# Performance work log

Measured on AMD Instinct MI355X. Metric: run time of the kernel, lower is better.

## Reference

```python
import jax, jax.numpy as jnp
import numpy as np

# ---- module hyperparameters (from init_kwargs) ----
KL_TEMP = 4.0
NUM_CLASSES = 100
POLICY_NUMS = 7          # linear out dim = POLICY_NUMS + 2 (identity, classes, policies)
FEATURE_NUMS = 128       # linear in dim = concat of two 64-d policy features
POS_W = (1.0, 0.5, 0.001)
NEG_W = (1.0, 0.5, 0.001)
KD_CE_W = (1.0, 1.0)
LOSS_W = (1.0, 1.0, 1.0)
BATCH = 2048


def setup_inputs() -> dict:
    key = jax.random.key(0)
    ks = jax.random.split(key, 9)
    O = POLICY_NUMS + 2
    return {
        "student_logits": jax.random.normal(ks[0], (BATCH, NUM_CLASSES), jnp.float32),
        "teacher_logits": jax.random.normal(ks[1], (BATCH, NUM_CLASSES), jnp.float32),
        "student_policy": jax.random.normal(ks[2], (BATCH, FEATURE_NUMS // 2), jnp.float32),
        "teacher_policy": jax.random.normal(ks[3], (BATCH, FEATURE_NUMS // 2), jnp.float32),
        "W1": jax.random.normal(ks[4], (O, FEATURE_NUMS), jnp.float32) * 0.08,  # frozen teacher linear
        "bias1": jax.random.normal(ks[5], (O,), jnp.float32) * 0.01,
        "W2": jax.random.normal(ks[6], (O, FEATURE_NUMS), jnp.float32) * 0.08,  # trainable student linear
        "bias2": jax.random.normal(ks[7], (O,), jnp.float32) * 0.01,
        "targets": jax.random.randint(ks[8], (BATCH, 1, POLICY_NUMS + 1), 0, 10, dtype=jnp.int32),
    }


def _kldiv_mean(inp, tgt):
    # torch KLDivLoss(reduction='mean'): mean over all elems of target*(log(target)-input), zero where target<=0
    safe = jnp.where(tgt > 0, tgt, 1.0)
    return jnp.where(tgt > 0, tgt * (jnp.log(safe) - inp), 0.0).mean()


def _wmean(loss, tgt, pw, nw):
    return jnp.where(tgt == 1.0, loss * pw, loss * nw).mean()


def _pair_linear(feat, W, bias):
    # L[i, j] = W @ concat(f_even[j], f_odd[i]) + bias, computed without materializing [b1,b1,2f]
    f = feat.shape[-1]
    f1, f2 = feat[0::2], feat[1::2]                       # [b1, f] each
    A = f1 @ W[:, :f].T                                   # [b1, O]  (j part)
    B = f2 @ W[:, f:].T                                   # [b1, O]  (i part)
    return B[:, None, :] + A[None, :, :] + bias           # [b1, b1, O]


def _policy_loss(teacher_policy, student_policy, targets, W1, bias1, W2, bias2):
    B = student_policy.shape[0]
    b1 = B // 2
    dt = student_policy.dtype

    Ls = _pair_linear(student_policy, W2, bias2)          # [b1,b1,O]
    Lt = jax.lax.stop_gradient(_pair_linear(teacher_policy, W1, bias1))

    sI, sC = Ls[..., 0], Ls[..., 1]
    sP = Ls[..., 2:].reshape(b1 * b1, POLICY_NUMS)
    tI, tC = Lt[..., 0], Lt[..., 1]
    tP = Lt[..., 2:].reshape(b1 * b1, POLICY_NUMS)

    eye = jnp.eye(b1, dtype=dt)
    # off-diagonal identity entries are detached for the student (teacher already no-grad)
    sI = eye * sI + (1.0 - eye) * jax.lax.stop_gradient(sI)

    t = targets.reshape(B, POLICY_NUMS + 1)
    t1, t2 = t[0::2], t[1::2]
    Teq = (t1[None, :, :] == t2[:, None, :]).astype(dt)   # [b1,b1,P+1]

    classes_value = 1.0 / (NUM_CLASSES - 1) + 1.0
    identity_value = 1.0 / (b1 - 1) + 1.0
    gC = Teq[..., 0] * classes_value - 1.0 / (NUM_CLASSES - 1)
    gP = Teq[..., 1:].reshape(b1 * b1, POLICY_NUMS) * 2.0 - 1.0
    gI = eye * identity_value - 1.0 / (b1 - 1)

    kl_loss = (_wmean((sI - tI) ** 2, gI, POS_W[0], NEG_W[0])
               + _wmean((sC - tC) ** 2, gC, POS_W[1], NEG_W[1])
               + _wmean((sP - tP) ** 2, gP, POS_W[2], NEG_W[2]))

    # KLDivLoss(reduction='mean') returns a scalar; torch.where broadcasts it, so .mean() of weights scales it
    ce_loss = (_kldiv_mean(sI, gI) * jnp.where(gI == 1.0, POS_W[0], NEG_W[0]).mean()
               + _kldiv_mean(sC, gC) * jnp.where(gC == 1.0, POS_W[1], NEG_W[1]).mean()
               + _wmean((sP - gP) ** 2, gP, POS_W[2], NEG_W[2]))

    return KD_CE_W[0] * kl_loss + KD_CE_W[1] * ce_loss


def reference(student_logits, teacher_logits, student_policy, teacher_policy, W1, bias1, W2, bias2, targets):
    B = student_logits.shape[0]
    # ---- CE loss (targets last dim <= 15 -> integer class label at column 0) ----
    labels = targets.reshape(B, -1)[:, 0]
    logp = jax.nn.log_softmax(student_logits, axis=1)
    ce_loss = -jnp.take_along_axis(logp, labels[:, None], axis=1).mean()

    # ---- KD KL loss (KLDivLoss reduction='mean' over all elements) ----
    t_prob = jax.nn.softmax(teacher_logits / KL_TEMP, axis=1)
    s_logp = jax.nn.log_softmax(student_logits / KL_TEMP, axis=1)
    kl_loss = _kldiv_mean(s_logp, t_prob) * (KL_TEMP ** 2)

    # ---- pairwise policy loss (the fusion-heavy path) ----
    policy_loss = _policy_loss(teacher_policy, student_policy, targets, W1, bias1, W2, bias2)

    return LOSS_W[0] * ce_loss + LOSS_W[1] * kl_loss + LOSS_W[2] * policy_loss
```

## Files before the change

### kernel.cpp

```cpp
#include <hip/hip_runtime.h>
#include <math.h>

#define NCLS   100
#define BATCH_ 2048
#define OK     9
#define FHALF  64

#define NLOGB  128
#define NPOLB  16
#define NBLK   (NLOGB + NPOLB)

#define LP_OFF 0
#define PS_OFF (LP_OFF + NLOGB * 2)
#define PB_OFF (PS_OFF + NPOLB * 72)

__device__ __forceinline__ float waveSum(float v) {
#pragma unroll
    for (int off = 32; off; off >>= 1) v += __shfl_xor(v, off, 64);
    return v;
}
__device__ __forceinline__ float waveMax(float v) {
#pragma unroll
    for (int off = 32; off; off >>= 1) v = fmaxf(v, __shfl_xor(v, off, 64));
    return v;
}

__global__ __launch_bounds__(1024) void stats_kernel(
        const float* __restrict__ slog, const float* __restrict__ tlog,
        const float* __restrict__ spol, const float* __restrict__ tpol,
        const float* __restrict__ W1,   const float* __restrict__ W2,
        const int*   __restrict__ tgt,  float* __restrict__ ws)
{
    __shared__ float w1s[OK * 128];
    __shared__ float w2s[OK * 128];
    __shared__ float bkt[320];
    __shared__ float redL[32];

    const int tid  = threadIdx.x;
    const int wave = tid >> 6;
    const int lane = tid & 63;

    if (blockIdx.x < NLOGB) {
        const int r = blockIdx.x * 16 + wave;
        const float* x = slog + r * NCLS;
        const float* y = tlog + r * NCLS;
        const int label = tgt[r * 8];
        const bool has2 = lane < (NCLS - 64);
        float x1 = x[lane];
        float y1 = y[lane];
        float x2 = has2 ? x[lane + 64] : -3.0e38f;
        float y2 = has2 ? y[lane + 64] : -3.0e38f;
        float xl = x[label];
        float mx = waveMax(fmaxf(x1, x2));
        float my = waveMax(fmaxf(y1, y2));
        float se1  = waveSum(expf(x1 - mx) + (has2 ? expf(x2 - mx) : 0.f));
        float se4s = waveSum(expf((x1 - mx) * 0.25f) + (has2 ? expf((x2 - mx) * 0.25f) : 0.f));
        float e1 = expf((y1 - my) * 0.25f);
        float e2 = has2 ? expf((y2 - my) * 0.25f) : 0.f;
        float se4t = waveSum(e1 + e2);
        float tnum = waveSum(e1 * (y1 - x1) * 0.25f + (has2 ? e2 * (y2 - x2) * 0.25f : 0.f));
        if (lane == 0) {
            float logZ1  = mx + logf(se1);
            float logZ4s = mx * 0.25f + logf(se4s);
            float logZ4t = my * 0.25f + logf(se4t);
            redL[wave * 2]     = logZ1 - xl;
            redL[wave * 2 + 1] = tnum / se4t + logZ4s - logZ4t;
        }
        __syncthreads();
        if (tid < 2) {
            float s = 0.f;
#pragma unroll
            for (int w = 0; w < 16; ++w) s += redL[w * 2 + tid];
            ws[LP_OFF + blockIdx.x * 2 + tid] = s;
        }
    } else {
        const int pb = blockIdx.x - NLOGB;
        for (int idx = tid; idx < OK * 128; idx += 1024) { w1s[idx] = W1[idx]; w2s[idx] = W2[idx]; }
        if (tid < 320) bkt[tid] = 0.f;
        __syncthreads();

        float As[OK], Bs[OK];
        if (tid < 64) {
            const int i = pb * 64 + tid;
            const float4* f1s = (const float4*)(spol + (2 * i) * FHALF);
            const float4* f2s = (const float4*)(spol + (2 * i + 1) * FHALF);
            const float4* f1t = (const float4*)(tpol + (2 * i) * FHALF);
            const float4* f2t = (const float4*)(tpol + (2 * i + 1) * FHALF);

            float At[OK], Bt[OK];
#pragma unroll
            for (int k = 0; k < OK; ++k) { As[k] = 0.f; Bs[k] = 0.f; At[k] = 0.f; Bt[k] = 0.f; }
            for (int f4 = 0; f4 < FHALF / 4; ++f4) {
                float4 a4 = f1s[f4], b4 = f2s[f4], c4 = f1t[f4], d4 = f2t[f4];
                const float* ap = (const float*)&a4;
                const float* bp = (const float*)&b4;
                const float* cp = (const float*)&c4;
                const float* dp = (const float*)&d4;
#pragma unroll
                for (int j = 0; j < 4; ++j) {
                    const int f = f4 * 4 + j;
                    const float av = ap[j], bv = bp[j], cv = cp[j], dv = dp[j];
#pragma unroll
                    for (int k = 0; k < OK; ++k) {
                        As[k] = fmaf(av, w2s[k * 128 + f],      As[k]);
                        Bs[k] = fmaf(bv, w2s[k * 128 + 64 + f], Bs[k]);
                        At[k] = fmaf(cv, w1s[k * 128 + f],      At[k]);
                        Bt[k] = fmaf(dv, w1s[k * 128 + 64 + f], Bt[k]);
                    }
                }
            }

#pragma unroll
            for (int k = 0; k < OK; ++k) {
                float du = Bs[k] - Bt[k], dw = As[k] - At[k];
                float v0 = waveSum(du),     v1 = waveSum(du * du);
                float v2 = waveSum(dw),     v3 = waveSum(dw * dw);
                float v4 = waveSum(Bs[k]),  v5 = waveSum(Bs[k] * Bs[k]);
                float v6 = waveSum(As[k]),  v7 = waveSum(As[k] * As[k]);
                if (lane == 0) {
                    float* p = ws + PS_OFF + pb * 72 + k * 8;
                    p[0] = v0; p[1] = v1; p[2] = v2; p[3] = v3;
                    p[4] = v4; p[5] = v5; p[6] = v6; p[7] = v7;
                }
            }

            const int* t1r = tgt + (2 * i) * 8;
            const int* t2r = tgt + (2 * i + 1) * 8;
#pragma unroll
            for (int c0 = 0; c0 < 8; ++c0) {
                int v1i = t1r[c0], v2i = t2r[c0];
                atomicAdd(&bkt[0 * 80 + c0 * 10 + v1i], 1.0f);
                atomicAdd(&bkt[1 * 80 + c0 * 10 + v2i], 1.0f);
                atomicAdd(&bkt[2 * 80 + c0 * 10 + v1i], As[c0 + 1]);
                atomicAdd(&bkt[3 * 80 + c0 * 10 + v2i], Bs[c0 + 1]);
            }
        }
        __syncthreads();
        if (tid < 320) ws[PB_OFF + pb * 320 + tid] = bkt[tid];
    }
}

__global__ __launch_bounds__(256) void combine_kernel(
        const float* __restrict__ ws,
        const float* __restrict__ bias1, const float* __restrict__ bias2,
        float* __restrict__ out)
{
    __shared__ float statsC[72];
    __shared__ float bktC[320];
    __shared__ float cekl[8];

    const int tid  = threadIdx.x;
    const int wave = tid >> 6;
    const int lane = tid & 63;

    float ce = 0.f, kl = 0.f;
    if (tid < NLOGB) {
        ce = ws[LP_OFF + tid * 2];
        kl = ws[LP_OFF + tid * 2 + 1];
    }
    ce = waveSum(ce); kl = waveSum(kl);
    if (lane == 0) { cekl[wave * 2] = ce; cekl[wave * 2 + 1] = kl; }

    if (tid < 72) {
        float s = 0.f;
#pragma unroll
        for (int b = 0; b < NPOLB; ++b) s += ws[PS_OFF + b * 72 + tid];
        statsC[tid] = s;
    }
    for (int idx = tid; idx < 320; idx += 256) {
        float s = 0.f;
#pragma unroll
        for (int b = 0; b < NPOLB; ++b) s += ws[PB_OFF + b * 320 + idx];
        bktC[idx] = s;
    }
    __syncthreads();

    if (tid == 0) {
        const double N = 1024.0, M = 1048576.0;
        double ce_main = (double)(cekl[0] + cekl[2] + cekl[4] + cekl[6]) / (double)BATCH_;
        double kl_main = (double)(cekl[1] + cekl[3] + cekl[5] + cekl[7]) * 16.0
                       / (double)(BATCH_ * NCLS);

        double kl_pol = 0.0, Sp_acc = 0.0;
        double SumL[OK], SumL2[OK];
        for (int k = 0; k < OK; ++k) {
            const float* p = &statsC[k * 8];
            double D1u = p[0], D2u = p[1], D1w = p[2], D2w = p[3];
            double U1 = p[4], U2 = p[5], Wa1 = p[6], Wa2 = p[7];
            double cd = (double)bias2[k] - (double)bias1[k];
            double b  = (double)bias2[k];
            double S = N * D2u + N * (D2w + 2.0 * cd * D1w + N * cd * cd)
                     + 2.0 * D1u * (D1w + N * cd);
            if (k == 0)      kl_pol += S / M;
            else if (k == 1) kl_pol += 0.5 * S / M;
            else             Sp_acc += S;
            SumL[k]  = N * U1 + N * Wa1 + M * b;
            SumL2[k] = N * U2 + N * (Wa2 + 2.0 * b * Wa1 + N * b * b)
                     + 2.0 * U1 * (Wa1 + N * b);
        }
        kl_pol += 0.001 * Sp_acc / (7.0 * M);

        double ce_I = -((double)statsC[4] + (double)statsC[6] + N * (double)bias2[0]) / M;

        const float* cnt1 = &bktC[0];
        const float* cnt2 = &bktC[80];
        const float* sA   = &bktC[160];
        const float* sB   = &bktC[240];
        double ce_C = 0.0, ceP = 0.0;
        for (int c0 = 0; c0 < 8; ++c0) {
            double ms = 0.0, pc = 0.0;
            for (int v = 0; v < 10; ++v) {
                double c1 = (double)cnt1[c0 * 10 + v], c2 = (double)cnt2[c0 * 10 + v];
                ms += c1 * (double)sB[c0 * 10 + v] + c2 * (double)sA[c0 * 10 + v];
                pc += c1 * c2;
            }
            ms += (double)bias2[c0 + 1] * pc;
            if (c0 == 0) {
                ce_C = -0.5 * ms / M;
            } else {
                int k = c0 + 1;
                double sg = 2.0 * ms - SumL[k];
                ceP += SumL2[k] - 2.0 * sg + M;
            }
        }
        ceP *= 0.001 / (7.0 * M);

        out[0] = (float)(ce_main + kl_main + kl_pol + ce_I + ce_C + ceP);
    }
}

extern "C" void kernel_launch(void* const* d_in, const int* in_sizes, int n_in,
                              void* d_out, int out_size, void* d_ws, size_t ws_size,
                              hipStream_t stream) {
    const float* slog = (const float*)d_in[0];
    const float* tlog = (const float*)d_in[1];
    const float* spol = (const float*)d_in[2];
    const float* tpol = (const float*)d_in[3];
    const float* W1   = (const float*)d_in[4];
    const float* b1   = (const float*)d_in[5];
    const float* W2   = (const float*)d_in[6];
    const float* b2   = (const float*)d_in[7];
    const int*   tgt  = (const int*)d_in[8];
    float* ws = (float*)d_ws;

    stats_kernel<<<NBLK, 1024, 0, stream>>>(slog, tlog, spol, tpol, W1, W2, tgt, ws);
    combine_kernel<<<1, 256, 0, stream>>>(ws, b1, b2, (float*)d_out);
}
```

Baseline: 98.07 us.

## Shrink stats blocks to 256 threads and use all threads in policy blocks

Changes the stats kernel from 1024-thread to 256-thread blocks. Logit blocks go from 128 to 512 with four rows each, and policy blocks go from 16 to 4 with every thread computing a pair projection instead of only the first wave. Per-wave projection statistics are reduced in shared memory before the global write, and the combine kernel is adjusted for the larger number of logit partials. This removes the idle 960 threads per policy block and spreads the logit work over more CUs, at the cost of heavier shared-memory atomic contention per policy block.

```diff
diff --git a/kernel.cpp b/kernel.cpp
--- a/kernel.cpp
+++ b/kernel.cpp
@@ -6,8 +6,8 @@
 #define OK     9
 #define FHALF  64
 
-#define NLOGB  128
-#define NPOLB  16
+#define NLOGB  512
+#define NPOLB  4
 #define NBLK   (NLOGB + NPOLB)
 
 #define LP_OFF 0
@@ -25,7 +25,7 @@
     return v;
 }
 
-__global__ __launch_bounds__(1024) void stats_kernel(
+__global__ __launch_bounds__(256) void stats_kernel(
         const float* __restrict__ slog, const float* __restrict__ tlog,
         const float* __restrict__ spol, const float* __restrict__ tpol,
         const float* __restrict__ W1,   const float* __restrict__ W2,
@@ -34,14 +34,15 @@
     __shared__ float w1s[OK * 128];
     __shared__ float w2s[OK * 128];
     __shared__ float bkt[320];
-    __shared__ float redL[32];
+    __shared__ float statsW[4][72];
+    __shared__ float redL[8];
 
     const int tid  = threadIdx.x;
     const int wave = tid >> 6;
     const int lane = tid & 63;
 
     if (blockIdx.x < NLOGB) {
-        const int r = blockIdx.x * 16 + wave;
+        const int r = blockIdx.x * 4 + wave;
         const float* x = slog + r * NCLS;
         const float* y = tlog + r * NCLS;
         const int label = tgt[r * 8];
@@ -67,76 +68,74 @@
             redL[wave * 2 + 1] = tnum / se4t + logZ4s - logZ4t;
         }
         __syncthreads();
-        if (tid < 2) {
-            float s = 0.f;
-#pragma unroll
-            for (int w = 0; w < 16; ++w) s += redL[w * 2 + tid];
-            ws[LP_OFF + blockIdx.x * 2 + tid] = s;
-        }
+        if (tid < 2)
+            ws[LP_OFF + blockIdx.x * 2 + tid] =
+                redL[tid] + redL[2 + tid] + redL[4 + tid] + redL[6 + tid];
     } else {
         const int pb = blockIdx.x - NLOGB;
-        for (int idx = tid; idx < OK * 128; idx += 1024) { w1s[idx] = W1[idx]; w2s[idx] = W2[idx]; }
-        if (tid < 320) bkt[tid] = 0.f;
+        for (int idx = tid; idx < OK * 128; idx += 256) { w1s[idx] = W1[idx]; w2s[idx] = W2[idx]; }
+        for (int idx = tid; idx < 320; idx += 256) bkt[idx] = 0.f;
         __syncthreads();
 
-        float As[OK], Bs[OK];
-        if (tid < 64) {
-            const int i = pb * 64 + tid;
-            const float4* f1s = (const float4*)(spol + (2 * i) * FHALF);
-            const float4* f2s = (const float4*)(spol + (2 * i + 1) * FHALF);
-            const float4* f1t = (const float4*)(tpol + (2 * i) * FHALF);
-            const float4* f2t = (const float4*)(tpol + (2 * i + 1) * FHALF);
-
-            float At[OK], Bt[OK];
-#pragma unroll
-            for (int k = 0; k < OK; ++k) { As[k] = 0.f; Bs[k] = 0.f; At[k] = 0.f; Bt[k] = 0.f; }
-            for (int f4 = 0; f4 < FHALF / 4; ++f4) {
-                float4 a4 = f1s[f4], b4 = f2s[f4], c4 = f1t[f4], d4 = f2t[f4];
-                const float* ap = (const float*)&a4;
-                const float* bp = (const float*)&b4;
-                const float* cp = (const float*)&c4;
-                const float* dp = (const float*)&d4;
-#pragma unroll
-                for (int j = 0; j < 4; ++j) {
-                    const int f = f4 * 4 + j;
-                    const float av = ap[j], bv = bp[j], cv = cp[j], dv = dp[j];
-#pragma unroll
-                    for (int k = 0; k < OK; ++k) {
-                        As[k] = fmaf(av, w2s[k * 128 + f],      As[k]);
-                        Bs[k] = fmaf(bv, w2s[k * 128 + 64 + f], Bs[k]);
-                        At[k] = fmaf(cv, w1s[k * 128 + f],      At[k]);
-                        Bt[k] = fmaf(dv, w1s[k * 128 + 64 + f], Bt[k]);
-                    }
+        const int i = pb * 256 + tid;
+        const float4* f1s = (const float4*)(spol + (2 * i) * FHALF);
+        const float4* f2s = (const float4*)(spol + (2 * i + 1) * FHALF);
+        const float4* f1t = (const float4*)(tpol + (2 * i) * FHALF);
+        const float4* f2t = (const float4*)(tpol + (2 * i + 1) * FHALF);
+
+        float As[OK], Bs[OK], At[OK], Bt[OK];
+#pragma unroll
+        for (int k = 0; k < OK; ++k) { As[k] = 0.f; Bs[k] = 0.f; At[k] = 0.f; Bt[k] = 0.f; }
+        for (int f4 = 0; f4 < FHALF / 4; ++f4) {
+            float4 a4 = f1s[f4], b4 = f2s[f4], c4 = f1t[f4], d4 = f2t[f4];
+            const float* ap = (const float*)&a4;
+            const float* bp = (const float*)&b4;
+            const float* cp = (const float*)&c4;
+            const float* dp = (const float*)&d4;
+#pragma unroll
+            for (int j = 0; j < 4; ++j) {
+                const int f = f4 * 4 + j;
+                const float av = ap[j], bv = bp[j], cv = cp[j], dv = dp[j];
+#pragma unroll
+                for (int k = 0; k < OK; ++k) {
+                    As[k] = fmaf(av, w2s[k * 128 + f],      As[k]);
+                    Bs[k] = fmaf(bv, w2s[k * 128 + 64 + f], Bs[k]);
+                    At[k] = fmaf(cv, w1s[k * 128 + f],      At[k]);
+                    Bt[k] = fmaf(dv, w1s[k * 128 + 64 + f], Bt[k]);
                 }
             }
-
-#pragma unroll
-            for (int k = 0; k < OK; ++k) {
-                float du = Bs[k] - Bt[k], dw = As[k] - At[k];
-                float v0 = waveSum(du),     v1 = waveSum(du * du);
-                float v2 = waveSum(dw),     v3 = waveSum(dw * dw);
-                float v4 = waveSum(Bs[k]),  v5 = waveSum(Bs[k] * Bs[k]);
-                float v6 = waveSum(As[k]),  v7 = waveSum(As[k] * As[k]);
-                if (lane == 0) {
-                    float* p = ws + PS_OFF + pb * 72 + k * 8;
-                    p[0] = v0; p[1] = v1; p[2] = v2; p[3] = v3;
-                    p[4] = v4; p[5] = v5; p[6] = v6; p[7] = v7;
-                }
-            }
-
-            const int* t1r = tgt + (2 * i) * 8;
-            const int* t2r = tgt + (2 * i + 1) * 8;
-#pragma unroll
-            for (int c0 = 0; c0 < 8; ++c0) {
-                int v1i = t1r[c0], v2i = t2r[c0];
-                atomicAdd(&bkt[0 * 80 + c0 * 10 + v1i], 1.0f);
-                atomicAdd(&bkt[1 * 80 + c0 * 10 + v2i], 1.0f);
-                atomicAdd(&bkt[2 * 80 + c0 * 10 + v1i], As[c0 + 1]);
-                atomicAdd(&bkt[3 * 80 + c0 * 10 + v2i], Bs[c0 + 1]);
-            }
+        }
+
+#pragma unroll
+        for (int k = 0; k < OK; ++k) {
+            float du = Bs[k] - Bt[k], dw = As[k] - At[k];
+            float v0 = waveSum(du),     v1 = waveSum(du * du);
+            float v2 = waveSum(dw),     v3 = waveSum(dw * dw);
+            float v4 = waveSum(Bs[k]),  v5 = waveSum(Bs[k] * Bs[k]);
+            float v6 = waveSum(As[k]),  v7 = waveSum(As[k] * As[k]);
+            if (lane == 0) {
+                float* p = &statsW[wave][k * 8];
+                p[0] = v0; p[1] = v1; p[2] = v2; p[3] = v3;
+                p[4] = v4; p[5] = v5; p[6] = v6; p[7] = v7;
+            }
+        }
+
+        const int* t1r = tgt + (2 * i) * 8;
+        const int* t2r = tgt + (2 * i + 1) * 8;
+#pragma unroll
+        for (int c0 = 0; c0 < 8; ++c0) {
+            int v1i = t1r[c0], v2i = t2r[c0];
+            atomicAdd(&bkt[0 * 80 + c0 * 10 + v1i], 1.0f);
+            atomicAdd(&bkt[1 * 80 + c0 * 10 + v2i], 1.0f);
+            atomicAdd(&bkt[2 * 80 + c0 * 10 + v1i], As[c0 + 1]);
+            atomicAdd(&bkt[3 * 80 + c0 * 10 + v2i], Bs[c0 + 1]);
         }
         __syncthreads();
-        if (tid < 320) ws[PB_OFF + pb * 320 + tid] = bkt[tid];
+        if (tid < 72)
+            ws[PS_OFF + pb * 72 + tid] =
+                statsW[0][tid] + statsW[1][tid] + statsW[2][tid] + statsW[3][tid];
+        for (int idx = tid; idx < 320; idx += 256)
+            ws[PB_OFF + pb * 320 + idx] = bkt[idx];
     }
 }
 
@@ -154,9 +153,10 @@
     const int lane = tid & 63;
 
     float ce = 0.f, kl = 0.f;
-    if (tid < NLOGB) {
-        ce = ws[LP_OFF + tid * 2];
-        kl = ws[LP_OFF + tid * 2 + 1];
+#pragma unroll
+    for (int s = 0; s < NLOGB; s += 256) {
+        ce += ws[LP_OFF + (s + tid) * 2];
+        kl += ws[LP_OFF + (s + tid) * 2 + 1];
     }
     ce = waveSum(ce); kl = waveSum(kl);
     if (lane == 0) { cekl[wave * 2] = ce; cekl[wave * 2 + 1] = kl; }
@@ -243,6 +243,6 @@
     const int*   tgt  = (const int*)d_in[8];
     float* ws = (float*)d_ws;
 
-    stats_kernel<<<NBLK, 1024, 0, stream>>>(slog, tlog, spol, tpol, W1, W2, tgt, ws);
+    stats_kernel<<<NBLK, 256, 0, stream>>>(slog, tlog, spol, tpol, W1, W2, tgt, ws);
     combine_kernel<<<1, 256, 0, stream>>>(ws, b1, b2, (float*)d_out);
 }
```

Result: slower. 109.0 us (+11.2%).
